# Performance work log

Hardware: AMD Instinct MI355X
Metric: run time of the kernel (lower is better)

The kernel has to match this reference:

```python
import jax, jax.numpy as jnp
import numpy as np
import math

D_MODEL = 1024
N_HEADS = 16
HEAD_DIM = D_MODEL // N_HEADS  # 64
KV_DIM = 4 * HEAD_DIM          # 256
THETA = 10000.0
B, T = 2, 2048


def setup_inputs() -> dict:
    key = jax.random.key(0)
    ks = jax.random.split(key, 14)
    s = lambda k, *sh: jax.random.normal(k, sh, dtype=jnp.float32) * 0.02
    inp = {
        "x": jax.random.normal(ks[0], (B, T, D_MODEL), dtype=jnp.float32),
        "mask": jnp.tril(jnp.ones((T, T), dtype=jnp.int32))[None, None],  # causal [1,1,T,T]
        "Wq": s(ks[1], D_MODEL, D_MODEL), "bq": jnp.zeros((D_MODEL,), jnp.float32),
        "Wkv": s(ks[2], D_MODEL, KV_DIM), "bkv": jnp.zeros((KV_DIM,), jnp.float32),
        "Wk": s(ks[3], KV_DIM, D_MODEL), "bk": jnp.zeros((D_MODEL,), jnp.float32),
        "Wv": s(ks[4], KV_DIM, D_MODEL), "bv": jnp.zeros((D_MODEL,), jnp.float32),
        "Wo": s(ks[5], D_MODEL, D_MODEL), "bo": jnp.zeros((D_MODEL,), jnp.float32),
        "Wkr": s(ks[6], HEAD_DIM, HEAD_DIM),  # decoupled k_rope linear, no bias
    }
    return inp


def _rotate_half(x):
    x1, x2 = jnp.split(x, 2, axis=-1)
    return jnp.concatenate((-x2, x1), axis=-1)


def reference(x, mask, Wq, bq, Wkv, bkv, Wk, bk, Wv, bv, Wo, bo, Wkr):
    Bq, Tq, C = x.shape
    kv = x @ Wkv + bkv                                # [B,T,KV_DIM]
    k = (kv @ Wk + bk).reshape(Bq, Tq, N_HEADS, HEAD_DIM).transpose(0, 2, 1, 3)
    v = (kv @ Wv + bv).reshape(Bq, Tq, N_HEADS, HEAD_DIM).transpose(0, 2, 1, 3)
    q = (x @ Wq + bq).reshape(Bq, Tq, N_HEADS, HEAD_DIM).transpose(0, 2, 1, 3)

    # standard RoPE on q
    inv_freq = 1.0 / (THETA ** (jnp.arange(0, HEAD_DIM, 2, dtype=jnp.float32) / HEAD_DIM))
    t = jnp.arange(Tq, dtype=jnp.float32)
    freqs = t[:, None] * inv_freq[None, :]            # [T, D/2]
    emb = jnp.concatenate((freqs, freqs), axis=-1)    # [T, D]
    q = q * jnp.cos(emb) + _rotate_half(q) * jnp.sin(emb)

    # decoupled position path for k: scale by position index, then linear
    k = (k * t[None, None, :, None]) @ Wkr            # [B,H,T,D]

    attn = jnp.einsum('bhtd,bhsd->bhts', q, k) * (1.0 / math.sqrt(HEAD_DIM))
    attn = jnp.where(mask == 0, -jnp.inf, attn)
    attn = jax.nn.softmax(attn, axis=-1)
    y = jnp.einsum('bhts,bhsd->bhtd', attn, v)
    y = y.transpose(0, 2, 1, 3).reshape(Bq, Tq, C)
    return y @ Wo + bo
```

## Files before the change

kernel.cpp:

```cpp
#include <hip/hip_runtime.h>
#include <hip/hip_bf16.h>
#include <math.h>

typedef __bf16 bf16x8 __attribute__((ext_vector_type(8)));
typedef __bf16 bf16x4 __attribute__((ext_vector_type(4)));
typedef float  f32x4  __attribute__((ext_vector_type(4)));

#define T_SEQ 2048
#define NH    16
#define HD    64
#define DM    1024
#define QSCALE 0.18033688011112043f

__device__ __forceinline__ f32x4 mfma16(bf16x8 a, bf16x8 b, f32x4 c) {
    return __builtin_amdgcn_mfma_f32_16x16x32_bf16(a, b, c, 0, 0, 0);
}

__device__ __forceinline__ void gl2lds(const void* g, void* l) {
    __builtin_amdgcn_global_load_lds(
        (const __attribute__((address_space(1))) void*)g,
        (__attribute__((address_space(3))) void*)l, 16, 0, 0);
}

__device__ __forceinline__ void tsplit_body(const float* __restrict__ in,
                                            __bf16* __restrict__ oh, __bf16* __restrict__ ol,
                                            int K, int N, int n0, int k0, int SPLIT,
                                            float* tile )
{
    const int tid = threadIdx.x;
#pragma unroll
    for (int it = 0; it < 2; ++it) {
        int r = it * 32 + (tid >> 3), c8 = (tid & 7) * 8;
        f32x4 a0 = *(const f32x4*)&in[(size_t)(k0 + r) * N + n0 + c8];
        f32x4 a1 = *(const f32x4*)&in[(size_t)(k0 + r) * N + n0 + c8 + 4];
#pragma unroll
        for (int j = 0; j < 4; ++j) { tile[r * 65 + c8 + j] = a0[j]; tile[r * 65 + c8 + 4 + j] = a1[j]; }
    }
    __syncthreads();
    const int n = tid >> 2, kb = (tid & 3) * 16;
    bf16x8 h0, h1, l0, l1;
#pragma unroll
    for (int j = 0; j < 8; ++j) {
        float v0 = tile[(kb + j) * 65 + n], v1 = tile[(kb + 8 + j) * 65 + n];
        __bf16 hb0 = (__bf16)v0, hb1 = (__bf16)v1;
        h0[j] = hb0; h1[j] = hb1;
        if (SPLIT) { l0[j] = (__bf16)(v0 - (float)hb0); l1[j] = (__bf16)(v1 - (float)hb1); }
    }
    size_t o = (size_t)(n0 + n) * K + k0 + kb;
    *(bf16x8*)&oh[o] = h0; *(bf16x8*)&oh[o + 8] = h1;
    if (SPLIT) { *(bf16x8*)&ol[o] = l0; *(bf16x8*)&ol[o + 8] = l1; }
}

__global__ __launch_bounds__(256)
void prep(const float* __restrict__ x, const float* __restrict__ Wq,
          const float* __restrict__ Wkv, const float* __restrict__ Wv,
          const float* __restrict__ Wo, const float* __restrict__ Wk,
          const float* __restrict__ Wkr, const float* __restrict__ bk,
          __bf16* xh, __bf16* xl, __bf16* Wqt_h, __bf16* Wqt_l,
          __bf16* Wkvt_h, __bf16* Wkvt_l, __bf16* Wvt, __bf16* Wot,
          __bf16* W2th, __bf16* W2tl, float* b2)
{
    __shared__ float tile[64 * 65];
    const int g = blockIdx.x, tid = threadIdx.x;
    if (g < 2048) {
        size_t idx = ((size_t)g * 256 + tid) * 8;
        f32x4 a0 = *(const f32x4*)&x[idx];
        f32x4 a1 = *(const f32x4*)&x[idx + 4];
        bf16x8 h, l;
#pragma unroll
        for (int j = 0; j < 4; ++j) {
            __bf16 h0 = (__bf16)a0[j];
            h[j]     = h0; l[j]     = (__bf16)(a0[j] - (float)h0);
            __bf16 h1 = (__bf16)a1[j];
            h[4 + j] = h1; l[4 + j] = (__bf16)(a1[j] - (float)h1);
        }
        *(bf16x8*)&xh[idx] = h;
        *(bf16x8*)&xl[idx] = l;
    } else if (g < 2304) {
        int i = g - 2048;
        tsplit_body(Wq, Wqt_h, Wqt_l, 1024, 1024, (i & 15) * 64, (i >> 4) * 64, 1, tile);
    } else if (g < 2368) {
        int i = g - 2304;
        tsplit_body(Wkv, Wkvt_h, Wkvt_l, 1024, 256, (i & 3) * 64, (i >> 2) * 64, 1, tile);
    } else if (g < 2432) {
        int i = g - 2368;
        tsplit_body(Wv, Wvt, nullptr, 256, 1024, (i & 15) * 64, (i >> 4) * 64, 0, tile);
    } else if (g < 2688) {
        int i = g - 2432;
        tsplit_body(Wo, Wot, nullptr, 1024, 1024, (i & 15) * 64, (i >> 4) * 64, 0, tile);
    } else {
        int o    = (g - 2688) * 256 + tid;
        int rowk = o >> 10, col = o & 1023;
        int h = col >> 6, d = col & 63;
        float acc = 0.0f;
        if (rowk < 256) {
#pragma unroll 8
            for (int j = 0; j < 64; ++j)
                acc += Wk[(size_t)rowk * DM + h * HD + j] * Wkr[j * HD + d];
            __bf16 hb = (__bf16)acc;
            W2th[(size_t)col * 256 + rowk] = hb;
            W2tl[(size_t)col * 256 + rowk] = (__bf16)(acc - (float)hb);
        } else {
#pragma unroll 8
            for (int j = 0; j < 64; ++j)
                acc += bk[h * HD + j] * Wkr[j * HD + d];
            b2[col] = acc;
        }
    }
}

template <int DUALA, int DUALB, int OUTM, int EPI>
__device__ __forceinline__
void gemm_body(char* smem,
               const __bf16* __restrict__ Ahi, const __bf16* __restrict__ Alo,
               const __bf16* __restrict__ Bhi, const __bf16* __restrict__ Blo,
               const float* __restrict__ bias, void* __restrict__ Cp,
               void* __restrict__ Cp2, int m0, int n0, int N, int K)
{
    const int tid  = threadIdx.x;
    const int w    = tid >> 6;
    const int lane = tid & 63;
    const int l16  = lane & 15;
    const int quad = lane >> 4;
    const int wy   = w >> 1, wx = w & 1;

    f32x4 acc[4][4];
#pragma unroll
    for (int i = 0; i < 4; ++i)
#pragma unroll
        for (int j = 0; j < 4; ++j) acc[i][j] = (f32x4)0.0f;

    auto stage = [&](int k0, int buf) {
        char* bb = smem + buf * 32768;
#pragma unroll
        for (int i = 0; i < 2; ++i) {
            int s = i * 256 + tid, row = s >> 2, c8 = (s & 3) * 8;
            size_t aoff = (size_t)(m0 + row) * K + k0 + c8;
            size_t boff = (size_t)(n0 + row) * K + k0 + c8;
            char*  dst  = bb + (row * 32 + c8) * 2;
            gl2lds(&Ahi[aoff], dst);
            if (DUALA) gl2lds(&Alo[aoff], dst + 8192);
            gl2lds(&Bhi[boff], dst + 16384);
            if (DUALB) gl2lds(&Blo[boff], dst + 24576);
        }
    };

    stage(0, 0);
    const int J = K >> 5;
    for (int j = 0; j < J; ++j) {
        __syncthreads();
        if (j + 1 < J) stage((j + 1) << 5, (j + 1) & 1);

        const __bf16* Ah = (const __bf16*)(smem + (j & 1) * 32768);
        const __bf16* Al = Ah + 4096;
        const __bf16* Bh = Ah + 8192;
        const __bf16* Bl = Ah + 12288;

        bf16x8 bfh[4], bfl[4];
#pragma unroll
        for (int ct = 0; ct < 4; ++ct) {
            bfh[ct] = *(const bf16x8*)&Bh[(wx * 64 + ct * 16 + l16) * 32 + quad * 8];
            if (DUALB) bfl[ct] = *(const bf16x8*)&Bl[(wx * 64 + ct * 16 + l16) * 32 + quad * 8];
        }
#pragma unroll
        for (int mf = 0; mf < 4; ++mf) {
            bf16x8 ah = *(const bf16x8*)&Ah[(wy * 64 + mf * 16 + l16) * 32 + quad * 8];
            bf16x8 al;
            if (DUALA) al = *(const bf16x8*)&Al[(wy * 64 + mf * 16 + l16) * 32 + quad * 8];
#pragma unroll
            for (int ct = 0; ct < 4; ++ct) {
                acc[mf][ct] = mfma16(ah, bfh[ct], acc[mf][ct]);
                if (DUALA) acc[mf][ct] = mfma16(al, bfh[ct], acc[mf][ct]);
                if (DUALB) acc[mf][ct] = mfma16(ah, bfl[ct], acc[mf][ct]);
            }
        }
    }

    float bias_v[4];
#pragma unroll
    for (int ct = 0; ct < 4; ++ct)
        bias_v[ct] = bias ? bias[n0 + wx * 64 + ct * 16 + l16] : 0.0f;

    if (EPI == 1) {
        __bf16* Chi = (__bf16*)Cp;
        __bf16* Clo = (__bf16*)Cp2;
#pragma unroll
        for (int mf = 0; mf < 4; ++mf) {
#pragma unroll
            for (int r = 0; r < 4; ++r) {
                int   m = m0 + wy * 64 + mf * 16 + quad * 4 + r;
                float t = (float)(m & (T_SEQ - 1));
#pragma unroll
                for (int ct = 0; ct < 2; ++ct) {
                    int   d   = ct * 16 + l16;
                    float inv = powf(10000.0f, -(float)d * (1.0f / 32.0f));
                    float sv, cv;
                    sincosf(t * inv, &sv, &cv);
                    float lo = acc[mf][ct][r]     + bias_v[ct];
                    float hi = acc[mf][ct + 2][r] + bias_v[ct + 2];
                    float v0 = (lo * cv - hi * sv) * QSCALE;
                    float v1 = (hi * cv + lo * sv) * QSCALE;
                    size_t i0 = (size_t)m * N + n0 + wx * 64 + d;
                    size_t i1 = i0 + 32;
                    __bf16 h0 = (__bf16)v0, h1 = (__bf16)v1;
                    Chi[i0] = h0; Clo[i0] = (__bf16)(v0 - (float)h0);
                    Chi[i1] = h1; Clo[i1] = (__bf16)(v1 - (float)h1);
                }
            }
        }
    } else if (EPI == 3) {
        __syncthreads();
        __bf16* vt = (__bf16*)(smem + w * 9216);
#pragma unroll
        for (int mf = 0; mf < 4; ++mf)
#pragma unroll
            for (int ct = 0; ct < 4; ++ct)
#pragma unroll
                for (int r = 0; r < 4; ++r)
                    vt[(ct * 16 + l16) * 72 + mf * 16 + quad * 4 + r] =
                        (__bf16)(acc[mf][ct][r] + bias_v[ct]);
        const int bb   = m0 >> 11;
        const int head = (n0 + wx * 64) >> 6;
        const int bh   = bb * 16 + head;
        __bf16* out    = (__bf16*)Cp;
        size_t  gbase  = ((size_t)(bh * 64 + lane)) * T_SEQ + (m0 & (T_SEQ - 1)) + wy * 64;
#pragma unroll
        for (int j8 = 0; j8 < 8; ++j8)
            *(bf16x8*)&out[gbase + j8 * 8] = *(const bf16x8*)&vt[lane * 72 + j8 * 8];
    } else {
#pragma unroll
        for (int mf = 0; mf < 4; ++mf) {
#pragma unroll
            for (int r = 0; r < 4; ++r) {
                int   m     = m0 + wy * 64 + mf * 16 + quad * 4 + r;
                float scale = (EPI == 2) ? (float)(m & (T_SEQ - 1)) : 1.0f;
#pragma unroll
                for (int ct = 0; ct < 4; ++ct) {
                    float  v   = (acc[mf][ct][r] + bias_v[ct]) * scale;
                    size_t idx = (size_t)m * N + n0 + wx * 64 + ct * 16 + l16;
                    if (OUTM == 1)      ((float*)Cp)[idx]  = v;
                    else if (OUTM == 0) ((__bf16*)Cp)[idx] = (__bf16)v;
                    else {
                        __bf16 hb = (__bf16)v;
                        ((__bf16*)Cp)[idx]  = hb;
                        ((__bf16*)Cp2)[idx] = (__bf16)(v - (float)hb);
                    }
                }
            }
        }
    }
}

__global__ __launch_bounds__(256)
void gemm_qkv(const __bf16* xh, const __bf16* xl,
              const __bf16* Wqt_h, const __bf16* Wqt_l, const float* bq,
              __bf16* qhi, __bf16* qlo,
              const __bf16* Wkvt_h, const __bf16* Wkvt_l, const float* bkv,
              __bf16* kvhi, __bf16* kvlo)
{
    __shared__ __attribute__((aligned(16))) char smem[65536];
    const int m0 = blockIdx.y * 128;
    if (blockIdx.x < 2)
        gemm_body<1, 1, 2, 0>(smem, xh, xl, Wkvt_h, Wkvt_l, bkv, kvhi, kvlo,
                              m0, blockIdx.x * 128, 256, 1024);
    else
        gemm_body<1, 1, 2, 1>(smem, xh, xl, Wqt_h, Wqt_l, bq, qhi, qlo,
                              m0, (blockIdx.x - 2) * 128, 1024, 1024);
}

__global__ __launch_bounds__(256)
void gemm_kv2(const __bf16* kvhi, const __bf16* kvlo,
              const __bf16* W2th, const __bf16* W2tl, const float* b2,
              __bf16* khi, __bf16* klo,
              const __bf16* Wvt, const float* bv, __bf16* vtg)
{
    __shared__ __attribute__((aligned(16))) char smem[65536];
    const int m0 = blockIdx.y * 128;
    if (blockIdx.x < 8)
        gemm_body<1, 1, 2, 2>(smem, kvhi, kvlo, W2th, W2tl, b2, khi, klo,
                              m0, blockIdx.x * 128, 1024, 256);
    else
        gemm_body<1, 0, 0, 3>(smem, kvhi, kvlo, Wvt, Wvt, bv, vtg, nullptr,
                              m0, (blockIdx.x - 8) * 128, 1024, 256);
}

__global__ __launch_bounds__(256)
void gemm_o(const __bf16* ybb, const __bf16* Wot, const float* bo, float* out)
{
    __shared__ __attribute__((aligned(16))) char smem[65536];
    gemm_body<0, 0, 1, 0>(smem, ybb, ybb, Wot, Wot, bo, out, nullptr,
                          blockIdx.y * 128, blockIdx.x * 128, 1024, 1024);
}

#define PSP 72
__global__ __launch_bounds__(256, 2)
void attn_v9(const __bf16* __restrict__ qhi, const __bf16* __restrict__ qlo,
             const __bf16* __restrict__ khi, const __bf16* __restrict__ klo,
             const __bf16* __restrict__ vtg, __bf16* __restrict__ yb)
{
    __shared__ __attribute__((aligned(16))) __bf16 Kh2[2][64 * 64];
    __shared__ __attribute__((aligned(16))) __bf16 Kl2[2][64 * 64];
    __shared__ __attribute__((aligned(16))) __bf16 Vt2[2][64 * 64];
    __shared__ __attribute__((aligned(16))) __bf16 Pw[4][16 * PSP];

    const int tid  = threadIdx.x;
    const int w    = tid >> 6;
    const int lane = tid & 63;
    const int l16  = lane & 15;
    const int quad = lane >> 4;

    const int g  = blockIdx.x;
    const int bh = g & 31, a = g >> 5;
    const int b  = bh >> 4, h = bh & 15;

    const int sr0 = tid >> 3, sc = tid & 7;
    const int sw  = l16 & 7;

    auto stage = [&](int j0, int buf) {
#pragma unroll
        for (int it = 0; it < 2; ++it) {
            int r   = it * 32 + sr0;
            int c8g = sc ^ (r & 7);
            int d0  = it * 2048 + tid * 8;
            gl2lds(&khi[(size_t)(b * T_SEQ + j0 + r) * DM + h * HD + c8g * 8], &Kh2[buf][d0]);
            gl2lds(&klo[(size_t)(b * T_SEQ + j0 + r) * DM + h * HD + c8g * 8], &Kl2[buf][d0]);
            gl2lds(&vtg[(size_t)(bh * HD + r) * T_SEQ + j0 + c8g * 8],         &Vt2[buf][d0]);
        }
    };

    for (int ph = 0; ph < 2; ++ph) {
        const int u  = ph ? a : (31 - a);
        const int q0 = u * 64;

        bf16x8 qh[2], ql[2];
        {
            const int    qr   = q0 + 16 * w + l16;
            const size_t qoff = (size_t)(b * T_SEQ + qr) * DM + h * HD;
#pragma unroll
            for (int s = 0; s < 2; ++s) {
                qh[s] = *(const bf16x8*)&qhi[qoff + s * 32 + quad * 8];
                ql[s] = *(const bf16x8*)&qlo[qoff + s * 32 + quad * 8];
            }
        }

        f32x4 o[4];
#pragma unroll
        for (int i = 0; i < 4; ++i) o[i] = (f32x4)0.0f;
        float m_i = -1e30f, l_i = 0.f;

        __syncthreads();
        stage(0, 0);

        for (int j0 = 0; j0 <= q0; j0 += 64) {
            const int  cur = (j0 >> 6) & 1;
            __syncthreads();
            if (j0 + 64 <= q0) stage(j0 + 64, cur ^ 1);

            const __bf16* Kh = Kh2[cur];
            const __bf16* Kl = Kl2[cur];
            const __bf16* Vt = Vt2[cur];

            f32x4 sa[4];
#pragma unroll
            for (int i = 0; i < 4; ++i) sa[i] = (f32x4)0.0f;
#pragma unroll
            for (int s = 0; s < 2; ++s) {
                const int c8s = ((s * 4 + quad) ^ sw) * 8;
#pragma unroll
                for (int kc = 0; kc < 4; ++kc) {
                    bf16x8 kh = *(const bf16x8*)&Kh[(kc * 16 + l16) * 64 + c8s];
                    bf16x8 kv = *(const bf16x8*)&Kl[(kc * 16 + l16) * 64 + c8s];
                    sa[kc] = mfma16(kh, qh[s], sa[kc]);
                    sa[kc] = mfma16(kv, qh[s], sa[kc]);
                    sa[kc] = mfma16(kh, ql[s], sa[kc]);
                }
            }

            const int  qr   = q0 + 16 * w + l16;
            const bool need = (j0 + 63 > q0 + 16 * w);
            if (need) {
#pragma unroll
                for (int kc = 0; kc < 4; ++kc)
#pragma unroll
                    for (int r = 0; r < 4; ++r)
                        if (j0 + kc * 16 + quad * 4 + r > qr) sa[kc][r] = -1e30f;
            }
            float mx = -1e30f;
#pragma unroll
            for (int kc = 0; kc < 4; ++kc)
#pragma unroll
                for (int r = 0; r < 4; ++r) mx = fmaxf(mx, sa[kc][r]);
            mx = fmaxf(mx, __shfl_xor(mx, 16));
            mx = fmaxf(mx, __shfl_xor(mx, 32));
            float mn    = fmaxf(fmaxf(m_i, mx), -1e20f);
            float alpha = exp2f(m_i - mn);
            m_i = mn;
            float rs = 0.f;
            __bf16* pw = &Pw[w][0];
#pragma unroll
            for (int kc = 0; kc < 4; ++kc) {
                float p0 = exp2f(sa[kc][0] - mn);
                float p1 = exp2f(sa[kc][1] - mn);
                float p2 = exp2f(sa[kc][2] - mn);
                float p3 = exp2f(sa[kc][3] - mn);
                rs += (p0 + p1) + (p2 + p3);
                bf16x4 pk = { (__bf16)p0, (__bf16)p1, (__bf16)p2, (__bf16)p3 };
                *(bf16x4*)&pw[l16 * PSP + kc * 16 + quad * 4] = pk;
            }
            rs += __shfl_xor(rs, 16);
            rs += __shfl_xor(rs, 32);
            l_i = l_i * alpha + rs;
#pragma unroll
            for (int dc = 0; dc < 4; ++dc) o[dc] *= alpha;

#pragma unroll
            for (int s = 0; s < 2; ++s) {
                const int c8s = ((s * 4 + quad) ^ sw) * 8;
                bf16x8 pb = *(const bf16x8*)&pw[l16 * PSP + s * 32 + quad * 8];
#pragma unroll
                for (int dc = 0; dc < 4; ++dc) {
                    bf16x8 va = *(const bf16x8*)&Vt[(dc * 16 + l16) * 64 + c8s];
                    o[dc] = mfma16(va, pb, o[dc]);
                }
            }
        }

        {
            float   invl = 1.0f / l_i;
            __bf16* pw   = &Pw[w][0];
#pragma unroll
            for (int dc = 0; dc < 4; ++dc) {
                bf16x4 ov = { (__bf16)(o[dc][0] * invl), (__bf16)(o[dc][1] * invl),
                              (__bf16)(o[dc][2] * invl), (__bf16)(o[dc][3] * invl) };
                *(bf16x4*)&pw[l16 * PSP + dc * 16 + quad * 4] = ov;
            }
            const int qrl  = lane >> 2;
            const int dch  = (lane & 3) * 16;
            const int qrow = q0 + 16 * w + qrl;
            const __bf16* src = &pw[qrl * PSP + dch];
            __bf16*       dst = &yb[(size_t)(b * T_SEQ + qrow) * DM + h * HD + dch];
            *(bf16x8*)dst       = *(const bf16x8*)src;
            *(bf16x8*)(dst + 8) = *(const bf16x8*)(src + 8);
        }
    }
}

extern "C" void kernel_launch(void* const* d_in, const int* in_sizes, int n_in,
                              void* d_out, int out_size, void* d_ws, size_t ws_size,
                              hipStream_t stream)
{
    (void)in_sizes; (void)n_in; (void)out_size; (void)ws_size;

    const float* x   = (const float*)d_in[0];
    const float* Wq  = (const float*)d_in[2];
    const float* bq  = (const float*)d_in[3];
    const float* Wkv = (const float*)d_in[4];
    const float* bkv = (const float*)d_in[5];
    const float* Wk  = (const float*)d_in[6];
    const float* bk  = (const float*)d_in[7];
    const float* Wv  = (const float*)d_in[8];
    const float* bv  = (const float*)d_in[9];
    const float* Wo  = (const float*)d_in[10];
    const float* bo  = (const float*)d_in[11];
    const float* Wkr = (const float*)d_in[12];

    const int    BT = 2 * T_SEQ;
    const size_t MB = 1024 * 1024;
    char* base = (char*)d_ws;

    __bf16* xhi    = (__bf16*)(base +  0 * MB);
    __bf16* xlo    = (__bf16*)(base +  8 * MB);
    __bf16* qhi    = (__bf16*)(base + 16 * MB);
    __bf16* qlo    = (__bf16*)(base + 24 * MB);
    __bf16* Wqt_h  = (__bf16*)(base + 32 * MB);
    __bf16* Wqt_l  = (__bf16*)(base + 34 * MB);
    __bf16* Wkvt_h = (__bf16*)(base + 36 * MB);
    __bf16* Wkvt_l = (__bf16*)(base + 37 * MB);
    __bf16* kvhi   = (__bf16*)(base + 38 * MB);
    __bf16* kvlo   = (__bf16*)(base + 40 * MB);
    __bf16* W2t_h  = (__bf16*)(base + 42 * MB);
    __bf16* W2t_l  = (__bf16*)(base + 42 * MB + 512 * 1024);
    __bf16* Wvt    = (__bf16*)(base + 43 * MB);
    __bf16* Wot    = (__bf16*)(base + 43 * MB + 512 * 1024);
    float*  b2     = (float*) (base + 45 * MB + 512 * 1024);
    __bf16* vtg    = (__bf16*)(base +  8 * MB);
    __bf16* ybb    = (__bf16*)(base +  0 * MB);
    __bf16* khi    = (__bf16*)d_out;
    __bf16* klo    = (__bf16*)d_out + (size_t)BT * DM;

    dim3 blk(256);
    prep<<<3716, blk, 0, stream>>>(x, Wq, Wkv, Wv, Wo, Wk, Wkr, bk,
                                   xhi, xlo, Wqt_h, Wqt_l, Wkvt_h, Wkvt_l,
                                   Wvt, Wot, W2t_h, W2t_l, b2);
    gemm_qkv<<<dim3(10, 32), blk, 0, stream>>>(xhi, xlo, Wqt_h, Wqt_l, bq, qhi, qlo,
                                               Wkvt_h, Wkvt_l, bkv, kvhi, kvlo);
    gemm_kv2<<<dim3(16, 32), blk, 0, stream>>>(kvhi, kvlo, W2t_h, W2t_l, b2,
                                               khi, klo, Wvt, bv, vtg);
    attn_v9<<<512, blk, 0, stream>>>(qhi, qlo, khi, klo, vtg, ybb);
    gemm_o<<<dim3(8, 32), blk, 0, stream>>>(ybb, Wot, bo, (float*)d_out);
}
```

Measured before the change: 257.8 us.

## Process paired causal query tiles together sharing each staged K/V tile

Instead of running the two balanced query tiles (31-a and a) one after another, each with its own pass over K/V, the attention kernel now keeps both tiles' Q fragments and accumulators in registers. It streams the K/V tiles once for the longer tile and also applies them to the shorter tile while it is still within range. This is meant to roughly halve global-to-LDS staging traffic and barriers for the shared prefix. In exchange it doubles register pressure for accumulators, Q and score fragments, which could cause spills or lower occupancy under the 2-blocks-per-CU launch bound, and it uses more LDS for the P scratch buffers.

Measured after the change: 271.5 us. +5.3%, slower.

```diff
diff --git a/kernel.cpp b/kernel.cpp
--- a/kernel.cpp
+++ b/kernel.cpp
@@ -294,14 +294,14 @@
 
 #define PSP 72
 __global__ __launch_bounds__(256, 2)
-void attn_v9(const __bf16* __restrict__ qhi, const __bf16* __restrict__ qlo,
-             const __bf16* __restrict__ khi, const __bf16* __restrict__ klo,
-             const __bf16* __restrict__ vtg, __bf16* __restrict__ yb)
+void attn_v10(const __bf16* __restrict__ qhi, const __bf16* __restrict__ qlo,
+              const __bf16* __restrict__ khi, const __bf16* __restrict__ klo,
+              const __bf16* __restrict__ vtg, __bf16* __restrict__ yb)
 {
     __shared__ __attribute__((aligned(16))) __bf16 Kh2[2][64 * 64];
     __shared__ __attribute__((aligned(16))) __bf16 Kl2[2][64 * 64];
     __shared__ __attribute__((aligned(16))) __bf16 Vt2[2][64 * 64];
-    __shared__ __attribute__((aligned(16))) __bf16 Pw[4][16 * PSP];
+    __shared__ __attribute__((aligned(16))) __bf16 Pw[4][2][16 * PSP];
 
     const int tid  = threadIdx.x;
     const int w    = tid >> 6;
@@ -312,6 +312,9 @@
     const int g  = blockIdx.x;
     const int bh = g & 31, a = g >> 5;
     const int b  = bh >> 4, h = bh & 15;
+
+    const int q0A = (31 - a) * 64;
+    const int q0B = a * 64;
 
     const int sr0 = tid >> 3, sc = tid & 7;
     const int sw  = l16 & 7;
@@ -328,120 +331,133 @@
         }
     };
 
-    for (int ph = 0; ph < 2; ++ph) {
-        const int u  = ph ? a : (31 - a);
-        const int q0 = u * 64;
-
-        bf16x8 qh[2], ql[2];
-        {
-            const int    qr   = q0 + 16 * w + l16;
-            const size_t qoff = (size_t)(b * T_SEQ + qr) * DM + h * HD;
-#pragma unroll
-            for (int s = 0; s < 2; ++s) {
-                qh[s] = *(const bf16x8*)&qhi[qoff + s * 32 + quad * 8];
-                ql[s] = *(const bf16x8*)&qlo[qoff + s * 32 + quad * 8];
-            }
-        }
-
-        f32x4 o[4];
-#pragma unroll
-        for (int i = 0; i < 4; ++i) o[i] = (f32x4)0.0f;
-        float m_i = -1e30f, l_i = 0.f;
-
+    bf16x8 qhA[2], qlA[2], qhB[2], qlB[2];
+    {
+        const size_t offA = (size_t)(b * T_SEQ + q0A + 16 * w + l16) * DM + h * HD;
+        const size_t offB = (size_t)(b * T_SEQ + q0B + 16 * w + l16) * DM + h * HD;
+#pragma unroll
+        for (int s = 0; s < 2; ++s) {
+            qhA[s] = *(const bf16x8*)&qhi[offA + s * 32 + quad * 8];
+            qlA[s] = *(const bf16x8*)&qlo[offA + s * 32 + quad * 8];
+            qhB[s] = *(const bf16x8*)&qhi[offB + s * 32 + quad * 8];
+            qlB[s] = *(const bf16x8*)&qlo[offB + s * 32 + quad * 8];
+        }
+    }
+
+    f32x4 oA[4], oB[4];
+#pragma unroll
+    for (int i = 0; i < 4; ++i) { oA[i] = (f32x4)0.0f; oB[i] = (f32x4)0.0f; }
+    float mA = -1e30f, lA = 0.f, mB = -1e30f, lB = 0.f;
+
+    stage(0, 0);
+
+    auto softmax = [&](f32x4* sa, float& m_i, float& l_i, f32x4* o,
+                       __bf16* pw, int q0f, int j0) {
+        const int  qr   = q0f + 16 * w + l16;
+        const bool need = (j0 + 63 > q0f + 16 * w);
+        if (need) {
+#pragma unroll
+            for (int kc = 0; kc < 4; ++kc)
+#pragma unroll
+                for (int r = 0; r < 4; ++r)
+                    if (j0 + kc * 16 + quad * 4 + r > qr) sa[kc][r] = -1e30f;
+        }
+        float mx = -1e30f;
+#pragma unroll
+        for (int kc = 0; kc < 4; ++kc)
+#pragma unroll
+            for (int r = 0; r < 4; ++r) mx = fmaxf(mx, sa[kc][r]);
+        mx = fmaxf(mx, __shfl_xor(mx, 16));
+        mx = fmaxf(mx, __shfl_xor(mx, 32));
+        float mn    = fmaxf(fmaxf(m_i, mx), -1e20f);
+        float alpha = exp2f(m_i - mn);
+        m_i = mn;
+        float rs = 0.f;
+#pragma unroll
+        for (int kc = 0; kc < 4; ++kc) {
+            float p0 = exp2f(sa[kc][0] - mn);
+            float p1 = exp2f(sa[kc][1] - mn);
+            float p2 = exp2f(sa[kc][2] - mn);
+            float p3 = exp2f(sa[kc][3] - mn);
+            rs += (p0 + p1) + (p2 + p3);
+            bf16x4 pk = { (__bf16)p0, (__bf16)p1, (__bf16)p2, (__bf16)p3 };
+            *(bf16x4*)&pw[l16 * PSP + kc * 16 + quad * 4] = pk;
+        }
+        rs += __shfl_xor(rs, 16);
+        rs += __shfl_xor(rs, 32);
+        l_i = l_i * alpha + rs;
+#pragma unroll
+        for (int dc = 0; dc < 4; ++dc) o[dc] *= alpha;
+    };
+
+    for (int j0 = 0; j0 <= q0A; j0 += 64) {
+        const int  cur  = (j0 >> 6) & 1;
+        const bool actB = (j0 <= q0B);
         __syncthreads();
-        stage(0, 0);
-
-        for (int j0 = 0; j0 <= q0; j0 += 64) {
-            const int  cur = (j0 >> 6) & 1;
-            __syncthreads();
-            if (j0 + 64 <= q0) stage(j0 + 64, cur ^ 1);
-
-            const __bf16* Kh = Kh2[cur];
-            const __bf16* Kl = Kl2[cur];
-            const __bf16* Vt = Vt2[cur];
-
-            f32x4 sa[4];
-#pragma unroll
-            for (int i = 0; i < 4; ++i) sa[i] = (f32x4)0.0f;
-#pragma unroll
-            for (int s = 0; s < 2; ++s) {
-                const int c8s = ((s * 4 + quad) ^ sw) * 8;
-#pragma unroll
-                for (int kc = 0; kc < 4; ++kc) {
-                    bf16x8 kh = *(const bf16x8*)&Kh[(kc * 16 + l16) * 64 + c8s];
-                    bf16x8 kv = *(const bf16x8*)&Kl[(kc * 16 + l16) * 64 + c8s];
-                    sa[kc] = mfma16(kh, qh[s], sa[kc]);
-                    sa[kc] = mfma16(kv, qh[s], sa[kc]);
-                    sa[kc] = mfma16(kh, ql[s], sa[kc]);
+        if (j0 + 64 <= q0A) stage(j0 + 64, cur ^ 1);
+
+        const __bf16* Kh = Kh2[cur];
+        const __bf16* Kl = Kl2[cur];
+        const __bf16* Vt = Vt2[cur];
+
+        f32x4 saA[4], saB[4];
+#pragma unroll
+        for (int i = 0; i < 4; ++i) { saA[i] = (f32x4)0.0f; saB[i] = (f32x4)0.0f; }
+#pragma unroll
+        for (int s = 0; s < 2; ++s) {
+            const int c8s = ((s * 4 + quad) ^ sw) * 8;
+#pragma unroll
+            for (int kc = 0; kc < 4; ++kc) {
+                bf16x8 kh = *(const bf16x8*)&Kh[(kc * 16 + l16) * 64 + c8s];
+                bf16x8 kv = *(const bf16x8*)&Kl[(kc * 16 + l16) * 64 + c8s];
+                saA[kc] = mfma16(kh, qhA[s], saA[kc]);
+                saA[kc] = mfma16(kv, qhA[s], saA[kc]);
+                saA[kc] = mfma16(kh, qlA[s], saA[kc]);
+                if (actB) {
+                    saB[kc] = mfma16(kh, qhB[s], saB[kc]);
+                    saB[kc] = mfma16(kv, qhB[s], saB[kc]);
+                    saB[kc] = mfma16(kh, qlB[s], saB[kc]);
                 }
             }
-
-            const int  qr   = q0 + 16 * w + l16;
-            const bool need = (j0 + 63 > q0 + 16 * w);
-            if (need) {
-#pragma unroll
-                for (int kc = 0; kc < 4; ++kc)
-#pragma unroll
-                    for (int r = 0; r < 4; ++r)
-                        if (j0 + kc * 16 + quad * 4 + r > qr) sa[kc][r] = -1e30f;
+        }
+
+        softmax(saA, mA, lA, oA, &Pw[w][0][0], q0A, j0);
+        if (actB) softmax(saB, mB, lB, oB, &Pw[w][1][0], q0B, j0);
+
+#pragma unroll
+        for (int s = 0; s < 2; ++s) {
+            const int c8s = ((s * 4 + quad) ^ sw) * 8;
+            bf16x8 pbA = *(const bf16x8*)&Pw[w][0][l16 * PSP + s * 32 + quad * 8];
+            bf16x8 pbB;
+            if (actB) pbB = *(const bf16x8*)&Pw[w][1][l16 * PSP + s * 32 + quad * 8];
+#pragma unroll
+            for (int dc = 0; dc < 4; ++dc) {
+                bf16x8 va = *(const bf16x8*)&Vt[(dc * 16 + l16) * 64 + c8s];
+                oA[dc] = mfma16(va, pbA, oA[dc]);
+                if (actB) oB[dc] = mfma16(va, pbB, oB[dc]);
             }
-            float mx = -1e30f;
-#pragma unroll
-            for (int kc = 0; kc < 4; ++kc)
-#pragma unroll
-                for (int r = 0; r < 4; ++r) mx = fmaxf(mx, sa[kc][r]);
-            mx = fmaxf(mx, __shfl_xor(mx, 16));
-            mx = fmaxf(mx, __shfl_xor(mx, 32));
-            float mn    = fmaxf(fmaxf(m_i, mx), -1e20f);
-            float alpha = exp2f(m_i - mn);
-            m_i = mn;
-            float rs = 0.f;
-            __bf16* pw = &Pw[w][0];
-#pragma unroll
-            for (int kc = 0; kc < 4; ++kc) {
-                float p0 = exp2f(sa[kc][0] - mn);
-                float p1 = exp2f(sa[kc][1] - mn);
-                float p2 = exp2f(sa[kc][2] - mn);
-                float p3 = exp2f(sa[kc][3] - mn);
-                rs += (p0 + p1) + (p2 + p3);
-                bf16x4 pk = { (__bf16)p0, (__bf16)p1, (__bf16)p2, (__bf16)p3 };
-                *(bf16x4*)&pw[l16 * PSP + kc * 16 + quad * 4] = pk;
-            }
-            rs += __shfl_xor(rs, 16);
-            rs += __shfl_xor(rs, 32);
-            l_i = l_i * alpha + rs;
-#pragma unroll
-            for (int dc = 0; dc < 4; ++dc) o[dc] *= alpha;
-
-#pragma unroll
-            for (int s = 0; s < 2; ++s) {
-                const int c8s = ((s * 4 + quad) ^ sw) * 8;
-                bf16x8 pb = *(const bf16x8*)&pw[l16 * PSP + s * 32 + quad * 8];
-#pragma unroll
-                for (int dc = 0; dc < 4; ++dc) {
-                    bf16x8 va = *(const bf16x8*)&Vt[(dc * 16 + l16) * 64 + c8s];
-                    o[dc] = mfma16(va, pb, o[dc]);
-                }
-            }
-        }
-
-        {
-            float   invl = 1.0f / l_i;
-            __bf16* pw   = &Pw[w][0];
-#pragma unroll
-            for (int dc = 0; dc < 4; ++dc) {
-                bf16x4 ov = { (__bf16)(o[dc][0] * invl), (__bf16)(o[dc][1] * invl),
-                              (__bf16)(o[dc][2] * invl), (__bf16)(o[dc][3] * invl) };
-                *(bf16x4*)&pw[l16 * PSP + dc * 16 + quad * 4] = ov;
-            }
-            const int qrl  = lane >> 2;
-            const int dch  = (lane & 3) * 16;
-            const int qrow = q0 + 16 * w + qrl;
-            const __bf16* src = &pw[qrl * PSP + dch];
-            __bf16*       dst = &yb[(size_t)(b * T_SEQ + qrow) * DM + h * HD + dch];
-            *(bf16x8*)dst       = *(const bf16x8*)src;
-            *(bf16x8*)(dst + 8) = *(const bf16x8*)(src + 8);
-        }
+        }
+    }
+
+#pragma unroll
+    for (int f = 0; f < 2; ++f) {
+        const f32x4* o    = f ? oB : oA;
+        const float  invl = 1.0f / (f ? lB : lA);
+        const int    q0f  = f ? q0B : q0A;
+        __bf16* pw = &Pw[w][f][0];
+#pragma unroll
+        for (int dc = 0; dc < 4; ++dc) {
+            bf16x4 ov = { (__bf16)(o[dc][0] * invl), (__bf16)(o[dc][1] * invl),
+                          (__bf16)(o[dc][2] * invl), (__bf16)(o[dc][3] * invl) };
+            *(bf16x4*)&pw[l16 * PSP + dc * 16 + quad * 4] = ov;
+        }
+        const int qrl  = lane >> 2;
+        const int dch  = (lane & 3) * 16;
+        const int qrow = q0f + 16 * w + qrl;
+        const __bf16* src = &pw[qrl * PSP + dch];
+        __bf16*       dst = &yb[(size_t)(b * T_SEQ + qrow) * DM + h * HD + dch];
+        *(bf16x8*)dst       = *(const bf16x8*)src;
+        *(bf16x8*)(dst + 8) = *(const bf16x8*)(src + 8);
     }
 }
 
@@ -496,6 +512,6 @@
                                                Wkvt_h, Wkvt_l, bkv, kvhi, kvlo);
     gemm_kv2<<<dim3(16, 32), blk, 0, stream>>>(kvhi, kvlo, W2t_h, W2t_l, b2,
                                                khi, klo, Wvt, bv, vtg);
-    attn_v9<<<512, blk, 0, stream>>>(qhi, qlo, khi, klo, vtg, ybb);
+    attn_v10<<<512, blk, 0, stream>>>(qhi, qlo, khi, klo, vtg, ybb);
     gemm_o<<<dim3(8, 32), blk, 0, stream>>>(ybb, Wot, bo, (float*)d_out);
 }
```
